# Kernel optimization log

Measured on AMD Instinct MI355X. Metric: run time of the kernel, lower is better.

The kernel has to match this reference:

```python
import jax, jax.numpy as jnp
import numpy as np

N_EX, N_IN, T = 256, 128, 512
H = 256  # n_out; gate dim = 4*H = 1024
W_SCALE = 0.05  # keep gates out of deep saturation


def setup_inputs() -> dict:
    key = jax.random.key(0)
    k1, k2, k3, k4 = jax.random.split(key, 4)
    X = jax.random.normal(k1, (N_EX, N_IN, T), dtype=jnp.float32)
    W_ih = jax.random.normal(k2, (4 * H, N_IN), dtype=jnp.float32) * W_SCALE
    W_hh = jax.random.normal(k3, (4 * H, H), dtype=jnp.float32) * W_SCALE
    b = jax.random.normal(k4, (4 * H,), dtype=jnp.float32) * W_SCALE
    return {"X": X, "W_ih": W_ih, "W_hh": W_hh, "b": b}


def reference(X, W_ih, W_hh, b):
    # Faithful to torch.nn.LSTMCell with bias_ih == bias_hh == b, gate order (i, f, g, o),
    # unrolled over timesteps with zero initial (h, c). Returns stacked hidden states A
    # and cell states C, each [T, n_ex, n_out] (matching the per-step lists A[1:], C[1:]).
    n_ex = X.shape[0]
    h_dim = W_hh.shape[1]
    # Precompute input projections for all timesteps: [T, n_ex, 4H]
    xt = jnp.transpose(X, (2, 0, 1))                      # [T, n_ex, n_in]
    x_proj = jnp.einsum('tbi,gi->tbg', xt, W_ih) + 2.0 * b

    def step(carry, xp):
        h, c = carry
        gates = xp + h @ W_hh.T                            # [n_ex, 4H]
        i, f, g, o = jnp.split(gates, 4, axis=-1)
        i = jax.nn.sigmoid(i)
        f = jax.nn.sigmoid(f)
        g = jnp.tanh(g)
        o = jax.nn.sigmoid(o)
        c_new = f * c + i * g
        h_new = o * jnp.tanh(c_new)
        return (h_new, c_new), (h_new, c_new)

    init = (jnp.zeros((n_ex, h_dim), X.dtype), jnp.zeros((n_ex, h_dim), X.dtype))
    _, (A, C) = jax.lax.scan(step, init, x_proj)
    return A, C
```

## Files before the change

### kernel.cpp

```cpp
#include <hip/hip_runtime.h>
#include <hip/hip_bf16.h>

#define TSTEPS 512
#define NEX 256
#define NIN 128
#define HDIM 256
#define NCOLS 16
#define NROWBLK 16

typedef __attribute__((ext_vector_type(8))) short short8;
typedef __attribute__((ext_vector_type(4))) float f32x4;
typedef __attribute__((ext_vector_type(4))) int i32x4;

__device__ __forceinline__ float sig_(float x) {
    return __builtin_amdgcn_rcpf(1.0f + __builtin_amdgcn_exp2f(-1.44269504f * x));
}
__device__ __forceinline__ float tanh_(float x) {
    return 1.0f - 2.0f * __builtin_amdgcn_rcpf(1.0f + __builtin_amdgcn_exp2f(2.88539008f * x));
}

__global__ void zero_ws(unsigned int* p, int n) {
    int i = blockIdx.x * blockDim.x + threadIdx.x;
    if (i < n) p[i] = 0u;
}

__global__ __launch_bounds__(64) void pack_x(const float* __restrict__ X,
                                             unsigned short* __restrict__ xp) {
    __shared__ __align__(16) unsigned short Ls[16][136];
    const int tid = threadIdx.x;
    const int ex = blockIdx.x >> 5;
    const int t0 = (blockIdx.x & 31) * 16;
#pragma unroll
    for (int s = 0; s < 8; ++s) {
        const int idx = s * 64 + tid;
        const int ii = idx >> 2, tq = idx & 3;
        const float4 v = *(const float4*)(X + ((size_t)ex * NIN + ii) * TSTEPS + t0 + tq * 4);
        const int o = ((ii >> 3) & 3) * 32 + (ii >> 5) * 8 + (ii & 7);
        __hip_bfloat16 b0 = (__hip_bfloat16)v.x, b1 = (__hip_bfloat16)v.y,
                       b2 = (__hip_bfloat16)v.z, b3 = (__hip_bfloat16)v.w;
        Ls[tq * 4 + 0][o] = *(unsigned short*)&b0;
        Ls[tq * 4 + 1][o] = *(unsigned short*)&b1;
        Ls[tq * 4 + 2][o] = *(unsigned short*)&b2;
        Ls[tq * 4 + 3][o] = *(unsigned short*)&b3;
    }
    __syncthreads();
#pragma unroll
    for (int s = 0; s < 4; ++s) {
        const int idx = s * 64 + tid;
        const int tl = idx >> 4, c = idx & 15;
        const short8 v = *(const short8*)&Ls[tl][c * 8];
        *(short8*)(xp + ((size_t)(t0 + tl) * NEX + ex) * NIN + c * 8) = v;
    }
}

template<int PX>
__global__ __launch_bounds__(64, 1) void lstm_persist(
    const float* __restrict__ X,
    const float* __restrict__ Wih,
    const float* __restrict__ Whh,
    const float* __restrict__ bias,
    float* __restrict__ A,
    float* __restrict__ C,
    char* __restrict__ hbuf2,
    const unsigned short* __restrict__ xp)
{
    __shared__ __align__(16) __hip_bfloat16 Ws[4][16][392];

    const int tid = threadIdx.x;
    const int b = blockIdx.x;
    const int i = b >> 4, j = b & 15;
    const int u0 = i * 16, e0 = j * 16;

    for (int idx = tid; idx < 64 * 96; idx += 64) {
        const int row = idx / 96, q = idx - row * 96;
        const int g = row >> 4, ul = row & 15;
        float4 v;
        int k0;
        if (q < 64) {
            v = *(const float4*)(Whh + (size_t)(g * HDIM + u0 + ul) * HDIM + 4 * q);
            k0 = 4 * q;
        } else {
            v = *(const float4*)(Wih + (size_t)(g * HDIM + u0 + ul) * NIN + 4 * (q - 64));
            k0 = HDIM + 4 * (q - 64);
        }
        Ws[g][ul][k0 + 0] = (__hip_bfloat16)v.x;
        Ws[g][ul][k0 + 1] = (__hip_bfloat16)v.y;
        Ws[g][ul][k0 + 2] = (__hip_bfloat16)v.z;
        Ws[g][ul][k0 + 3] = (__hip_bfloat16)v.w;
    }
    __syncthreads();

    const int mrow = tid & 15;
    const int kg   = tid >> 4;
    const int ex   = e0 + mrow;
    const int ub   = u0 + kg * 4;

    short8 wf0[12], wf1[12], wf2[12], wf3[12];
#pragma unroll
    for (int kk = 0; kk < 12; ++kk) {
        wf0[kk] = *(const short8*)&Ws[0][mrow][kk * 32 + kg * 8];
        wf1[kk] = *(const short8*)&Ws[1][mrow][kk * 32 + kg * 8];
        wf2[kk] = *(const short8*)&Ws[2][mrow][kk * 32 + kg * 8];
        wf3[kk] = *(const short8*)&Ws[3][mrow][kk * 32 + kg * 8];
    }
    float bsr[4][4];
#pragma unroll
    for (int g = 0; g < 4; ++g)
#pragma unroll
        for (int r = 0; r < 4; ++r)
            bsr[g][r] = 2.0f * bias[g * HDIM + ub + r];

    const f32x4 Z4 = {0.f, 0.f, 0.f, 0.f};
    float cr[4] = {0.f, 0.f, 0.f, 0.f};

    const size_t cons_off = (size_t)ex * 1024 + (size_t)kg * 32;
    const size_t prod_off = (size_t)ex * 1024 + (size_t)(i * 4 + kg) * 16;

#define X_GATHER(dst, tt)                                                          \
    {                                                                              \
        const float* xb = X + (size_t)ex * NIN * TSTEPS + (tt);                    \
        _Pragma("unroll")                                                          \
        for (int kk = 0; kk < 4; ++kk) {                                           \
            union { __hip_bfloat16 hh[8]; short8 v; } uxx;                         \
            _Pragma("unroll")                                                      \
            for (int e = 0; e < 8; ++e)                                            \
                uxx.hh[e] = (__hip_bfloat16)xb[(size_t)(kk * 32 + kg * 8 + e) * TSTEPS]; \
            (dst)[kk] = uxx.v;                                                     \
        }                                                                          \
    }

    for (int t = 0; t < TSTEPS; ++t) {
        short8 xf[4];
        if (PX) {
            const unsigned short* xrow = xp + ((size_t)t * NEX + ex) * NIN + kg * 32;
#pragma unroll
            for (int kk = 0; kk < 4; ++kk) xf[kk] = *(const short8*)(xrow + kk * 8);
        } else {
            X_GATHER(xf, t);
        }

        f32x4 a0 = Z4, a1 = Z4, a2 = Z4, a3 = Z4;

        if (t > 0) {
            const char* sb = hbuf2 + (size_t)((t - 1) & 1) * (NEX * 64 * 16) + cons_off;
            union Msg { i32x4 i4; unsigned int u[4]; } m[16];
            int rounds = 0;
            for (;;) {
                asm volatile(
                    "global_load_dwordx4 %0, %16, off sc0 sc1\n\t"
                    "global_load_dwordx4 %1, %16, off offset:16 sc0 sc1\n\t"
                    "global_load_dwordx4 %2, %16, off offset:128 sc0 sc1\n\t"
                    "global_load_dwordx4 %3, %16, off offset:144 sc0 sc1\n\t"
                    "global_load_dwordx4 %4, %16, off offset:256 sc0 sc1\n\t"
                    "global_load_dwordx4 %5, %16, off offset:272 sc0 sc1\n\t"
                    "global_load_dwordx4 %6, %16, off offset:384 sc0 sc1\n\t"
                    "global_load_dwordx4 %7, %16, off offset:400 sc0 sc1\n\t"
                    "global_load_dwordx4 %8, %16, off offset:512 sc0 sc1\n\t"
                    "global_load_dwordx4 %9, %16, off offset:528 sc0 sc1\n\t"
                    "global_load_dwordx4 %10, %16, off offset:640 sc0 sc1\n\t"
                    "global_load_dwordx4 %11, %16, off offset:656 sc0 sc1\n\t"
                    "global_load_dwordx4 %12, %16, off offset:768 sc0 sc1\n\t"
                    "global_load_dwordx4 %13, %16, off offset:784 sc0 sc1\n\t"
                    "global_load_dwordx4 %14, %16, off offset:896 sc0 sc1\n\t"
                    "global_load_dwordx4 %15, %16, off offset:912 sc0 sc1\n\t"
                    "s_waitcnt vmcnt(0)"
                    : "=&v"(m[0].i4), "=&v"(m[1].i4), "=&v"(m[2].i4), "=&v"(m[3].i4),
                      "=&v"(m[4].i4), "=&v"(m[5].i4), "=&v"(m[6].i4), "=&v"(m[7].i4),
                      "=&v"(m[8].i4), "=&v"(m[9].i4), "=&v"(m[10].i4), "=&v"(m[11].i4),
                      "=&v"(m[12].i4), "=&v"(m[13].i4), "=&v"(m[14].i4), "=&v"(m[15].i4)
                    : "v"(sb) : "memory");
                unsigned int mn = m[0].u[1] < m[0].u[3] ? m[0].u[1] : m[0].u[3];
#pragma unroll
                for (int q = 1; q < 16; ++q) {
                    const unsigned int lo = m[q].u[1] < m[q].u[3] ? m[q].u[1] : m[q].u[3];
                    mn = mn < lo ? mn : lo;
                }
                if (__all(mn == (unsigned int)t)) break;

                if (++rounds > 4096) {
                    for (;;) {
                        unsigned int mn2 = 0xFFFFFFFFu;
#pragma unroll
                        for (int q = 0; q < 16; ++q) {
                            const char* ms = sb + (q >> 1) * 128 + (q & 1) * 16;
                            const unsigned int t0v = __hip_atomic_load(
                                (const unsigned int*)(ms + 4),
                                __ATOMIC_RELAXED, __HIP_MEMORY_SCOPE_AGENT);
                            const unsigned int t1v = __hip_atomic_load(
                                (const unsigned int*)(ms + 12),
                                __ATOMIC_RELAXED, __HIP_MEMORY_SCOPE_AGENT);
                            const unsigned int lo = t0v < t1v ? t0v : t1v;
                            mn2 = mn2 < lo ? mn2 : lo;
                        }
                        if (__all(mn2 == (unsigned int)t)) break;
                    }
#pragma unroll
                    for (int q = 0; q < 16; ++q) {
                        const char* ms = sb + (q >> 1) * 128 + (q & 1) * 16;
                        m[q].u[0] = __hip_atomic_load((const unsigned int*)(ms + 0),
                                        __ATOMIC_RELAXED, __HIP_MEMORY_SCOPE_AGENT);
                        m[q].u[2] = __hip_atomic_load((const unsigned int*)(ms + 8),
                                        __ATOMIC_RELAXED, __HIP_MEMORY_SCOPE_AGENT);
                    }
                    break;
                }
            }
#pragma unroll
            for (int kk = 0; kk < 8; ++kk) {
                union { unsigned int u[4]; short8 v; } z;
                z.u[0] = m[2 * kk].u[0];
                z.u[1] = m[2 * kk].u[2];
                z.u[2] = m[2 * kk + 1].u[0];
                z.u[3] = m[2 * kk + 1].u[2];
                a0 = __builtin_amdgcn_mfma_f32_16x16x32_bf16(wf0[kk], z.v, a0, 0, 0, 0);
                a1 = __builtin_amdgcn_mfma_f32_16x16x32_bf16(wf1[kk], z.v, a1, 0, 0, 0);
                a2 = __builtin_amdgcn_mfma_f32_16x16x32_bf16(wf2[kk], z.v, a2, 0, 0, 0);
                a3 = __builtin_amdgcn_mfma_f32_16x16x32_bf16(wf3[kk], z.v, a3, 0, 0, 0);
            }
        }

#pragma unroll
        for (int kk = 0; kk < 4; ++kk) {
            a0 = __builtin_amdgcn_mfma_f32_16x16x32_bf16(wf0[8 + kk], xf[kk], a0, 0, 0, 0);
            a1 = __builtin_amdgcn_mfma_f32_16x16x32_bf16(wf1[8 + kk], xf[kk], a1, 0, 0, 0);
            a2 = __builtin_amdgcn_mfma_f32_16x16x32_bf16(wf2[8 + kk], xf[kk], a2, 0, 0, 0);
            a3 = __builtin_amdgcn_mfma_f32_16x16x32_bf16(wf3[8 + kk], xf[kk], a3, 0, 0, 0);
        }

        float hr[4];
#pragma unroll
        for (int r = 0; r < 4; ++r) {
            const float gi = sig_(a0[r] + bsr[0][r]);
            const float gf = sig_(a1[r] + bsr[1][r]);
            const float gg = tanh_(a2[r] + bsr[2][r]);
            const float go = sig_(a3[r] + bsr[3][r]);
            cr[r] = gf * cr[r] + gi * gg;
            hr[r] = go * tanh_(cr[r]);
        }

        union { unsigned int u[4]; i32x4 i4; } P;
        __hip_bfloat162 p01(__float2bfloat16(hr[0]), __float2bfloat16(hr[1]));
        __hip_bfloat162 p23(__float2bfloat16(hr[2]), __float2bfloat16(hr[3]));
        P.u[0] = *(unsigned int*)&p01;
        P.u[1] = (unsigned int)(t + 1);
        P.u[2] = *(unsigned int*)&p23;
        P.u[3] = (unsigned int)(t + 1);
        char* dst = hbuf2 + (size_t)(t & 1) * (NEX * 64 * 16) + prod_off;
        asm volatile("global_store_dwordx4 %0, %1, off sc0 sc1"
                     :: "v"(dst), "v"(P.i4) : "memory");

        const size_t off = (size_t)t * NEX * HDIM + (size_t)ex * HDIM + ub;
        *(float4*)&A[off] = make_float4(hr[0], hr[1], hr[2], hr[3]);
        *(float4*)&C[off] = make_float4(cr[0], cr[1], cr[2], cr[3]);
    }
#undef X_GATHER
}

extern "C" void kernel_launch(void* const* d_in, const int* in_sizes, int n_in,
                              void* d_out, int out_size, void* d_ws, size_t ws_size,
                              hipStream_t stream) {
    const float* X   = (const float*)d_in[0];
    const float* Wih = (const float*)d_in[1];
    const float* Whh = (const float*)d_in[2];
    const float* b   = (const float*)d_in[3];
    float* A = (float*)d_out;
    float* C = A + (size_t)TSTEPS * NEX * HDIM;

    const size_t hbuf_bytes = (size_t)2 * NEX * 64 * 16;
    const size_t xp_bytes   = (size_t)TSTEPS * NEX * NIN * sizeof(unsigned short);

    char* hbuf2 = (char*)d_ws;
    unsigned short* xpw = (unsigned short*)((char*)d_ws + hbuf_bytes);
    const bool px = ws_size >= hbuf_bytes + xp_bytes;

    const int nzero = (int)(hbuf_bytes / 4);
    zero_ws<<<(nzero + 255) / 256, 256, 0, stream>>>((unsigned int*)hbuf2, nzero);
    if (px) pack_x<<<dim3(NEX * 32), dim3(64), 0, stream>>>(X, xpw);

    const unsigned short* xpc = xpw;
    if (px) {
        void* args[] = {(void*)&X, (void*)&Wih, (void*)&Whh, (void*)&b,
                        (void*)&A, (void*)&C, (void*)&hbuf2, (void*)&xpc};
        hipError_t err = hipLaunchCooperativeKernel((const void*)lstm_persist<1>,
                                                    dim3(256), dim3(64), args, 0, stream);
        if (err != hipSuccess) {
            lstm_persist<1><<<dim3(256), dim3(64), 0, stream>>>(X, Wih, Whh, b, A, C, hbuf2, xpc);
        }
    } else {
        void* args[] = {(void*)&X, (void*)&Wih, (void*)&Whh, (void*)&b,
                        (void*)&A, (void*)&C, (void*)&hbuf2, (void*)&xpc};
        hipError_t err = hipLaunchCooperativeKernel((const void*)lstm_persist<0>,
                                                    dim3(256), dim3(64), args, 0, stream);
        if (err != hipSuccess) {
            lstm_persist<0><<<dim3(256), dim3(64), 0, stream>>>(X, Wih, Whh, b, A, C, hbuf2, xpc);
        }
    }
}
```

Baseline: 1.133 ms.

## Poll h-messages with lighter cache scope, prefetch next x, issue input MFMAs first

```diff
diff --git a/kernel.cpp b/kernel.cpp
--- a/kernel.cpp
+++ b/kernel.cpp
@@ -7,6 +7,7 @@
 #define HDIM 256
 #define NCOLS 16
 #define NROWBLK 16
+#define FASTLIM 2048
 
 typedef __attribute__((ext_vector_type(8))) short short8;
 typedef __attribute__((ext_vector_type(4))) float f32x4;
@@ -51,6 +52,70 @@
         const short8 v = *(const short8*)&Ls[tl][c * 8];
         *(short8*)(xp + ((size_t)(t0 + tl) * NEX + ex) * NIN + c * 8) = v;
     }
+}
+
+template<bool SYS>
+__device__ __forceinline__ void msg_load16(const char* sb, i32x4* mi) {
+    if (SYS) {
+        asm volatile(
+            "global_load_dwordx4 %0, %16, off sc0 sc1\n\t"
+            "global_load_dwordx4 %1, %16, off offset:16 sc0 sc1\n\t"
+            "global_load_dwordx4 %2, %16, off offset:128 sc0 sc1\n\t"
+            "global_load_dwordx4 %3, %16, off offset:144 sc0 sc1\n\t"
+            "global_load_dwordx4 %4, %16, off offset:256 sc0 sc1\n\t"
+            "global_load_dwordx4 %5, %16, off offset:272 sc0 sc1\n\t"
+            "global_load_dwordx4 %6, %16, off offset:384 sc0 sc1\n\t"
+            "global_load_dwordx4 %7, %16, off offset:400 sc0 sc1\n\t"
+            "global_load_dwordx4 %8, %16, off offset:512 sc0 sc1\n\t"
+            "global_load_dwordx4 %9, %16, off offset:528 sc0 sc1\n\t"
+            "global_load_dwordx4 %10, %16, off offset:640 sc0 sc1\n\t"
+            "global_load_dwordx4 %11, %16, off offset:656 sc0 sc1\n\t"
+            "global_load_dwordx4 %12, %16, off offset:768 sc0 sc1\n\t"
+            "global_load_dwordx4 %13, %16, off offset:784 sc0 sc1\n\t"
+            "global_load_dwordx4 %14, %16, off offset:896 sc0 sc1\n\t"
+            "global_load_dwordx4 %15, %16, off offset:912 sc0 sc1\n\t"
+            "s_waitcnt vmcnt(0)"
+            : "=&v"(mi[0]), "=&v"(mi[1]), "=&v"(mi[2]), "=&v"(mi[3]),
+              "=&v"(mi[4]), "=&v"(mi[5]), "=&v"(mi[6]), "=&v"(mi[7]),
+              "=&v"(mi[8]), "=&v"(mi[9]), "=&v"(mi[10]), "=&v"(mi[11]),
+              "=&v"(mi[12]), "=&v"(mi[13]), "=&v"(mi[14]), "=&v"(mi[15])
+            : "v"(sb) : "memory");
+    } else {
+        asm volatile(
+            "global_load_dwordx4 %0, %16, off sc0\n\t"
+            "global_load_dwordx4 %1, %16, off offset:16 sc0\n\t"
+            "global_load_dwordx4 %2, %16, off offset:128 sc0\n\t"
+            "global_load_dwordx4 %3, %16, off offset:144 sc0\n\t"
+            "global_load_dwordx4 %4, %16, off offset:256 sc0\n\t"
+            "global_load_dwordx4 %5, %16, off offset:272 sc0\n\t"
+            "global_load_dwordx4 %6, %16, off offset:384 sc0\n\t"
+            "global_load_dwordx4 %7, %16, off offset:400 sc0\n\t"
+            "global_load_dwordx4 %8, %16, off offset:512 sc0\n\t"
+            "global_load_dwordx4 %9, %16, off offset:528 sc0\n\t"
+            "global_load_dwordx4 %10, %16, off offset:640 sc0\n\t"
+            "global_load_dwordx4 %11, %16, off offset:656 sc0\n\t"
+            "global_load_dwordx4 %12, %16, off offset:768 sc0\n\t"
+            "global_load_dwordx4 %13, %16, off offset:784 sc0\n\t"
+            "global_load_dwordx4 %14, %16, off offset:896 sc0\n\t"
+            "global_load_dwordx4 %15, %16, off offset:912 sc0\n\t"
+            "s_waitcnt vmcnt(0)"
+            : "=&v"(mi[0]), "=&v"(mi[1]), "=&v"(mi[2]), "=&v"(mi[3]),
+              "=&v"(mi[4]), "=&v"(mi[5]), "=&v"(mi[6]), "=&v"(mi[7]),
+              "=&v"(mi[8]), "=&v"(mi[9]), "=&v"(mi[10]), "=&v"(mi[11]),
+              "=&v"(mi[12]), "=&v"(mi[13]), "=&v"(mi[14]), "=&v"(mi[15])
+            : "v"(sb) : "memory");
+    }
+}
+
+__device__ __forceinline__ unsigned int tagmin16(const i32x4* mi) {
+    const unsigned int* u = (const unsigned int*)mi;
+    unsigned int mn = 0xFFFFFFFFu;
+#pragma unroll
+    for (int q = 0; q < 16; ++q) {
+        const unsigned int lo = u[4 * q + 1] < u[4 * q + 3] ? u[4 * q + 1] : u[4 * q + 3];
+        mn = mn < lo ? mn : lo;
+    }
+    return mn;
 }
 
 template<int PX>
@@ -129,102 +194,57 @@
         }                                                                          \
     }
 
+    short8 xf[4];
+    if (PX) {
+        const unsigned short* xrow = xp + ((size_t)0 * NEX + ex) * NIN + kg * 32;
+#pragma unroll
+        for (int kk = 0; kk < 4; ++kk) xf[kk] = *(const short8*)(xrow + kk * 8);
+    } else {
+        X_GATHER(xf, 0);
+    }
+
+    bool sticky = false;
+
     for (int t = 0; t < TSTEPS; ++t) {
-        short8 xf[4];
-        if (PX) {
-            const unsigned short* xrow = xp + ((size_t)t * NEX + ex) * NIN + kg * 32;
-#pragma unroll
-            for (int kk = 0; kk < 4; ++kk) xf[kk] = *(const short8*)(xrow + kk * 8);
-        } else {
-            X_GATHER(xf, t);
-        }
-
         f32x4 a0 = Z4, a1 = Z4, a2 = Z4, a3 = Z4;
+#pragma unroll
+        for (int kk = 0; kk < 4; ++kk) {
+            a0 = __builtin_amdgcn_mfma_f32_16x16x32_bf16(wf0[8 + kk], xf[kk], a0, 0, 0, 0);
+            a1 = __builtin_amdgcn_mfma_f32_16x16x32_bf16(wf1[8 + kk], xf[kk], a1, 0, 0, 0);
+            a2 = __builtin_amdgcn_mfma_f32_16x16x32_bf16(wf2[8 + kk], xf[kk], a2, 0, 0, 0);
+            a3 = __builtin_amdgcn_mfma_f32_16x16x32_bf16(wf3[8 + kk], xf[kk], a3, 0, 0, 0);
+        }
 
         if (t > 0) {
             const char* sb = hbuf2 + (size_t)((t - 1) & 1) * (NEX * 64 * 16) + cons_off;
-            union Msg { i32x4 i4; unsigned int u[4]; } m[16];
-            int rounds = 0;
-            for (;;) {
-                asm volatile(
-                    "global_load_dwordx4 %0, %16, off sc0 sc1\n\t"
-                    "global_load_dwordx4 %1, %16, off offset:16 sc0 sc1\n\t"
-                    "global_load_dwordx4 %2, %16, off offset:128 sc0 sc1\n\t"
-                    "global_load_dwordx4 %3, %16, off offset:144 sc0 sc1\n\t"
-                    "global_load_dwordx4 %4, %16, off offset:256 sc0 sc1\n\t"
-                    "global_load_dwordx4 %5, %16, off offset:272 sc0 sc1\n\t"
-                    "global_load_dwordx4 %6, %16, off offset:384 sc0 sc1\n\t"
-                    "global_load_dwordx4 %7, %16, off offset:400 sc0 sc1\n\t"
-                    "global_load_dwordx4 %8, %16, off offset:512 sc0 sc1\n\t"
-                    "global_load_dwordx4 %9, %16, off offset:528 sc0 sc1\n\t"
-                    "global_load_dwordx4 %10, %16, off offset:640 sc0 sc1\n\t"
-                    "global_load_dwordx4 %11, %16, off offset:656 sc0 sc1\n\t"
-                    "global_load_dwordx4 %12, %16, off offset:768 sc0 sc1\n\t"
-                    "global_load_dwordx4 %13, %16, off offset:784 sc0 sc1\n\t"
-                    "global_load_dwordx4 %14, %16, off offset:896 sc0 sc1\n\t"
-                    "global_load_dwordx4 %15, %16, off offset:912 sc0 sc1\n\t"
-                    "s_waitcnt vmcnt(0)"
-                    : "=&v"(m[0].i4), "=&v"(m[1].i4), "=&v"(m[2].i4), "=&v"(m[3].i4),
-                      "=&v"(m[4].i4), "=&v"(m[5].i4), "=&v"(m[6].i4), "=&v"(m[7].i4),
-                      "=&v"(m[8].i4), "=&v"(m[9].i4), "=&v"(m[10].i4), "=&v"(m[11].i4),
-                      "=&v"(m[12].i4), "=&v"(m[13].i4), "=&v"(m[14].i4), "=&v"(m[15].i4)
-                    : "v"(sb) : "memory");
-                unsigned int mn = m[0].u[1] < m[0].u[3] ? m[0].u[1] : m[0].u[3];
-#pragma unroll
-                for (int q = 1; q < 16; ++q) {
-                    const unsigned int lo = m[q].u[1] < m[q].u[3] ? m[q].u[1] : m[q].u[3];
-                    mn = mn < lo ? mn : lo;
-                }
-                if (__all(mn == (unsigned int)t)) break;
-
-                if (++rounds > 4096) {
-                    for (;;) {
-                        unsigned int mn2 = 0xFFFFFFFFu;
-#pragma unroll
-                        for (int q = 0; q < 16; ++q) {
-                            const char* ms = sb + (q >> 1) * 128 + (q & 1) * 16;
-                            const unsigned int t0v = __hip_atomic_load(
-                                (const unsigned int*)(ms + 4),
-                                __ATOMIC_RELAXED, __HIP_MEMORY_SCOPE_AGENT);
-                            const unsigned int t1v = __hip_atomic_load(
-                                (const unsigned int*)(ms + 12),
-                                __ATOMIC_RELAXED, __HIP_MEMORY_SCOPE_AGENT);
-                            const unsigned int lo = t0v < t1v ? t0v : t1v;
-                            mn2 = mn2 < lo ? mn2 : lo;
-                        }
-                        if (__all(mn2 == (unsigned int)t)) break;
-                    }
-#pragma unroll
-                    for (int q = 0; q < 16; ++q) {
-                        const char* ms = sb + (q >> 1) * 128 + (q & 1) * 16;
-                        m[q].u[0] = __hip_atomic_load((const unsigned int*)(ms + 0),
-                                        __ATOMIC_RELAXED, __HIP_MEMORY_SCOPE_AGENT);
-                        m[q].u[2] = __hip_atomic_load((const unsigned int*)(ms + 8),
-                                        __ATOMIC_RELAXED, __HIP_MEMORY_SCOPE_AGENT);
-                    }
-                    break;
+            i32x4 m[16];
+            if (!sticky) {
+                int rounds = 0;
+                for (;;) {
+                    msg_load16<false>(sb, m);
+                    if (__all(tagmin16(m) == (unsigned int)t)) break;
+                    if (++rounds > FASTLIM) { sticky = true; break; }
                 }
             }
+            if (sticky) {
+                for (;;) {
+                    msg_load16<true>(sb, m);
+                    if (__all(tagmin16(m) == (unsigned int)t)) break;
+                }
+            }
+            const unsigned int* mu = (const unsigned int*)m;
 #pragma unroll
             for (int kk = 0; kk < 8; ++kk) {
                 union { unsigned int u[4]; short8 v; } z;
-                z.u[0] = m[2 * kk].u[0];
-                z.u[1] = m[2 * kk].u[2];
-                z.u[2] = m[2 * kk + 1].u[0];
-                z.u[3] = m[2 * kk + 1].u[2];
+                z.u[0] = mu[4 * (2 * kk) + 0];
+                z.u[1] = mu[4 * (2 * kk) + 2];
+                z.u[2] = mu[4 * (2 * kk + 1) + 0];
+                z.u[3] = mu[4 * (2 * kk + 1) + 2];
                 a0 = __builtin_amdgcn_mfma_f32_16x16x32_bf16(wf0[kk], z.v, a0, 0, 0, 0);
                 a1 = __builtin_amdgcn_mfma_f32_16x16x32_bf16(wf1[kk], z.v, a1, 0, 0, 0);
                 a2 = __builtin_amdgcn_mfma_f32_16x16x32_bf16(wf2[kk], z.v, a2, 0, 0, 0);
                 a3 = __builtin_amdgcn_mfma_f32_16x16x32_bf16(wf3[kk], z.v, a3, 0, 0, 0);
             }
-        }
-
-#pragma unroll
-        for (int kk = 0; kk < 4; ++kk) {
-            a0 = __builtin_amdgcn_mfma_f32_16x16x32_bf16(wf0[8 + kk], xf[kk], a0, 0, 0, 0);
-            a1 = __builtin_amdgcn_mfma_f32_16x16x32_bf16(wf1[8 + kk], xf[kk], a1, 0, 0, 0);
-            a2 = __builtin_amdgcn_mfma_f32_16x16x32_bf16(wf2[8 + kk], xf[kk], a2, 0, 0, 0);
-            a3 = __builtin_amdgcn_mfma_f32_16x16x32_bf16(wf3[8 + kk], xf[kk], a3, 0, 0, 0);
         }
 
         float hr[4];
@@ -246,12 +266,22 @@
         P.u[2] = *(unsigned int*)&p23;
         P.u[3] = (unsigned int)(t + 1);
         char* dst = hbuf2 + (size_t)(t & 1) * (NEX * 64 * 16) + prod_off;
-        asm volatile("global_store_dwordx4 %0, %1, off sc0 sc1"
+        asm volatile("global_store_dwordx4 %0, %1, off\n\t"
+                     "global_store_dwordx4 %0, %1, off sc0 sc1"
                      :: "v"(dst), "v"(P.i4) : "memory");
 
         const size_t off = (size_t)t * NEX * HDIM + (size_t)ex * HDIM + ub;
         *(float4*)&A[off] = make_float4(hr[0], hr[1], hr[2], hr[3]);
         *(float4*)&C[off] = make_float4(cr[0], cr[1], cr[2], cr[3]);
+        if (t + 1 < TSTEPS) {
+            if (PX) {
+                const unsigned short* xrow = xp + ((size_t)(t + 1) * NEX + ex) * NIN + kg * 32;
+#pragma unroll
+                for (int kk = 0; kk < 4; ++kk) xf[kk] = *(const short8*)(xrow + kk * 8);
+            } else {
+                X_GATHER(xf, t + 1);
+            }
+        }
     }
 #undef X_GATHER
 }
```

Result: slower. 2.312 ms (+104.1%).
